# Performance work log

Hardware: AMD Instinct MI355X
Metric: run time of the kernel (lower is better)

The kernel has to match this reference:

```python
import jax, jax.numpy as jnp
import numpy as np

BLANK = 0
NEG = -1e30  # finite -inf surrogate, safe for grads
LCAP = 512   # max decoded-hypothesis label length (static shape cap)


def _ctc_single(lp, labels, T_len, L_len):
    """CTC negative log-likelihood for one sequence.
    lp: [T, V] log-probs; labels: [L] padded int labels (blank=0 excluded).
    """
    T, V = lp.shape
    L = labels.shape[0]
    S = 2 * L + 1  # extended label seq: blank interleaved
    ext = jnp.zeros((S,), jnp.int32).at[1::2].set(labels)
    ext_m2 = jnp.concatenate([jnp.full((2,), -1, jnp.int32), ext[:-2]])
    skip = (ext != BLANK) & (ext != ext_m2)  # s-2 transition allowed
    lp_ext = lp[:, ext]  # [T, S]
    alpha0 = jnp.full((S,), NEG, lp.dtype)
    alpha0 = alpha0.at[0].set(lp_ext[0, 0]).at[1].set(lp_ext[0, 1])
    neg1 = jnp.full((1,), NEG, lp.dtype)
    neg2 = jnp.full((2,), NEG, lp.dtype)

    def step(alpha, inp):
        lp_t, t = inp
        a1 = jnp.concatenate([neg1, alpha[:-1]])
        a2 = jnp.where(skip, jnp.concatenate([neg2, alpha[:-2]]), NEG)
        new = jnp.logaddexp(jnp.logaddexp(alpha, a1), a2) + lp_t
        # freeze lattice past this sequence's true length
        return jnp.where(t < T_len, new, alpha), None

    alphaT, _ = jax.lax.scan(step, alpha0, (lp_ext[1:], jnp.arange(1, T)))
    end = jnp.logaddexp(alphaT[2 * L_len], alphaT[2 * L_len - 1])
    return -end


def _ctc_batch(acts, labels, act_lens, label_lens):
    lp = jax.nn.log_softmax(acts, axis=-1)   # [T, B, V]
    lp = jnp.transpose(lp, (1, 0, 2))        # [B, T, V]
    return jax.vmap(_ctc_single)(lp, labels, act_lens, label_lens)


def _greedy_decode(acts, act_lens):
    """Greedy CTC decode: argmax, collapse repeats, drop blanks. Static shapes."""
    T, B, V = acts.shape
    preds = jnp.argmax(acts, axis=-1).T.astype(jnp.int32)  # [B, T]
    prev = jnp.concatenate([jnp.full((B, 1), -1, jnp.int32), preds[:, :-1]], axis=1)
    tix = jnp.arange(T)[None, :]
    new_tok = (preds != BLANK) & (preds != prev) & (tix < act_lens[:, None])
    pos = jnp.cumsum(new_tok, axis=1) - 1
    keep = new_tok & (pos < LCAP)
    buf = jnp.zeros((B, LCAP + 1), jnp.int32)
    buf = buf.at[jnp.arange(B)[:, None], jnp.where(keep, pos, LCAP)].set(preds)
    dec = buf[:, :LCAP]
    dec_lens = jnp.maximum(jnp.minimum(new_tok.sum(axis=1), LCAP), 1).astype(jnp.int32)
    return dec, dec_lens


def setup_inputs() -> dict:
    key = jax.random.key(0)
    k1, k2, k3, k4 = jax.random.split(key, 4)
    T, B, V, L = 1500, 96, 128, 256
    acts = jax.random.normal(k1, (T, B, V), jnp.float32)
    labels = jax.random.randint(k2, (B, L), 1, V).astype(jnp.int32)
    act_lens = jax.random.randint(k3, (B,), 800, T + 1).astype(jnp.int32)
    label_lens = jax.random.randint(k4, (B,), 64, L + 1).astype(jnp.int32)
    return {"acts": acts, "labels": labels, "act_lens": act_lens, "label_lens": label_lens}


def reference(acts, labels, act_lens, label_lens):
    aug_loss = 1.0
    dec_labels, dec_lens = _greedy_decode(acts, act_lens)
    cost_gt = _ctc_batch(acts, labels, act_lens, label_lens)
    cost_hyp = _ctc_batch(acts, dec_labels, act_lens, dec_lens)
    return cost_gt - cost_hyp + aug_loss  # [B] per-utterance hinge costs
```

## Files before the change

kernel.cpp:

```cpp
#include <hip/hip_runtime.h>

#define TT 1500
#define BB 96
#define VV 128
#define LGT 256
#define LCAP 512
#define NEGF (-1.0e30f)
#define L2E 1.4426950408889634f
#define LN2F 0.6931471805599453f
#define NW 11
#define GH 34
#define HREF 16

__global__ __launch_bounds__(256) void decode_kernel(
    const float* __restrict__ acts, const int* __restrict__ act_lens,
    int* __restrict__ dec, int* __restrict__ dec_lens) {
  __shared__ int preds[TT];
  __shared__ int sc[256];
  const int b = blockIdx.x;
  const int tid = threadIdx.x;
  const int Tl = act_lens[b];
  for (int t = tid; t < Tl; t += 256) {
    const float4* r4 = (const float4*)(acts + ((size_t)t * BB + b) * VV);
    float best = -3.4e38f;
    int bi = 0;
#pragma unroll
    for (int i = 0; i < VV / 4; i++) {
      float4 v = r4[i];
      if (v.x > best) { best = v.x; bi = 4 * i; }
      if (v.y > best) { best = v.y; bi = 4 * i + 1; }
      if (v.z > best) { best = v.z; bi = 4 * i + 2; }
      if (v.w > best) { best = v.w; bi = 4 * i + 3; }
    }
    preds[t] = bi;
  }
  __syncthreads();

  int pv[6];
  bool fl[6];
  int cnt = 0;
#pragma unroll
  for (int j = 0; j < 6; j++) {
    int t = tid * 6 + j;
    bool valid = t < Tl;
    int p = valid ? preds[t] : 0;
    int pr = (t == 0) ? -1 : (valid ? preds[t - 1] : -1);
    bool f = valid && (p != 0) && (p != pr);
    pv[j] = p;
    fl[j] = f;
    cnt += f;
  }
  sc[tid] = cnt;
  __syncthreads();
  for (int off = 1; off < 256; off <<= 1) {
    int v = sc[tid];
    if (tid >= off) v += sc[tid - off];
    __syncthreads();
    sc[tid] = v;
    __syncthreads();
  }
  int pos = sc[tid] - cnt;
  int total = sc[255];
  int* db = dec + (size_t)b * LCAP;
#pragma unroll
  for (int j = 0; j < 6; j++) {
    if (fl[j]) {
      if (pos < LCAP) db[pos] = pv[j];
      pos++;
    }
  }
  if (tid == 0) {
    if (total == 0) db[0] = 0;
    dec_lens[b] = max(1, min(total, LCAP));
  }
}

__device__ __forceinline__ float shr1_negf(float x) {
  int r = __builtin_amdgcn_update_dpp(__float_as_int(NEGF), __float_as_int(x),
                                      0x138, 0xf, 0xf, false);
  return __int_as_float(r);
}

__device__ __forceinline__ float log1p2f(float x) {
  float w = __builtin_fmaf(x, 0.6666666666666666f, -0.3333333333333333f);
  float p = -0.16666666666666666f;
  p = __builtin_fmaf(p, w, 0.2f);
  p = __builtin_fmaf(p, w, -0.25f);
  p = __builtin_fmaf(p, w, 0.3333333333333333f);
  p = __builtin_fmaf(p, w, -0.5f);
  p = __builtin_fmaf(p, w, 1.0f);
  return __builtin_fmaf(p * w, L2E, 0.5849625007211562f);
}

__global__ __launch_bounds__(64 * NW, 1) void ctc_kernel(
    const float* __restrict__ acts, const int* __restrict__ labels_gt,
    const int* __restrict__ act_lens, const int* __restrict__ label_lens,
    const int* __restrict__ dec, const int* __restrict__ dec_lens,
    float* __restrict__ ends) {
  __shared__ float xall[2][2 * LCAP + 2];
  __shared__ float fin[2];
  const int b = blockIdx.x >> 1;
  const int hyp = blockIdx.x & 1;
  const int Tl = act_lens[b];
  const int len = hyp ? dec_lens[b] : label_lens[b];
  const int* lab = hyp ? (dec + (size_t)b * LCAP) : (labels_gt + (size_t)b * LGT);
  const int S = 2 * len + 1;
  const float* act_b = acts + (size_t)b * VV;
  const int Tlm1 = Tl - 1;

  const int tid = threadIdx.x;
  const int lane = tid & 63, wv = tid >> 6;
  const int oS = 2 * ((S + 2 * NW - 1) / (2 * NW));
  const int Se = (S + 1) & ~1;
  const int o0 = min(wv * oS, Se);
  const int o1 = min(o0 + oS, S);
  const int p0 = max(0, o0 - GH);
  const int s0 = p0 + 2 * lane;
  const int s1 = s0 + 1;

  int e1 = 0;
  bool skip = false;
  if (s1 < S) {
    int li = s1 >> 1;
    e1 = lab[li];
    if (s1 >= 3) skip = (e1 != 0) && (e1 != lab[li - 1]);
  }

  float a0 = NEGF, a1 = NEGF;
  if (wv == 0 && lane == 0) {
    a0 = act_b[0] * L2E;
    a1 = act_b[e1] * L2E;
  }

  float gL0, gL1, gL2, gL3, gL4, gL5, gL6, gL7;
  float gB0, gB1, gB2, gB3, gB4, gB5, gB6, gB7;

#define PREF(GL, GB, ROW)                                  \
  {                                                        \
    const float* rp_ = act_b + (size_t)(ROW) * (BB * VV);  \
    GB = rp_[0];                                           \
    GL = rp_[e1];                                          \
  }

#define STEPK(GL, GB)                                                     \
  {                                                                       \
    float pe = shr1_negf(a1);                                             \
                              \
    float m0 = fmaxf(a0, pe);                                             \
    float d0 = fminf(a0, pe) - m0;                                        \
    float u = m0 + log1p2f(__builtin_exp2f(d0));                          \
                                  \
    float w = skip ? u : a0;                                              \
    float m1 = fmaxf(a1, w);                                              \
    float d1 = fminf(a1, w) - m1;                                         \
    float v = m1 + log1p2f(__builtin_exp2f(d1));                          \
    a0 = __builtin_fmaf(GB, L2E, u);                                      \
    a1 = __builtin_fmaf(GL, L2E, v);                                      \
  }

#define REFRESH(K)                                       \
  {                                                      \
    float* xs = xall[(K)&1];                             \
    if (s0 >= o0 && s0 < o1) xs[s0] = a0;                \
    if (s1 >= o0 && s1 < o1) xs[s1] = a1;                \
    asm volatile("s_waitcnt lgkmcnt(0)" ::: "memory");   \
    __builtin_amdgcn_s_barrier();                        \
    if (s0 < o0) {                                       \
      a0 = xs[s0];                                       \
      a1 = (s1 < S) ? xs[s1] : NEGF;                     \
    }                                                    \
  }

#define W1(OFF, GL, GB)                    \
  STEPK(GL, GB);                           \
  PREF(GL, GB, min(t + (OFF) + 8, Tlm1));

#define T1(GL, GB)                         \
  STEPK(GL, GB);                           \
  PREF(GL, GB, min(t + 8, Tlm1));          \
  ++t;                                     \
  if (t >= Tl) break;

  PREF(gL0, gB0, min(1, Tlm1));
  PREF(gL1, gB1, min(2, Tlm1));
  PREF(gL2, gB2, min(3, Tlm1));
  PREF(gL3, gB3, min(4, Tlm1));
  PREF(gL4, gB4, min(5, Tlm1));
  PREF(gL5, gB5, min(6, Tlm1));
  PREF(gL6, gB6, min(7, Tlm1));
  PREF(gL7, gB7, min(8, Tlm1));

  int t = 1, k = 0;
  while (t + HREF <= Tl) {
    W1(0, gL0, gB0)
    W1(1, gL1, gB1)
    W1(2, gL2, gB2)
    W1(3, gL3, gB3)
    W1(4, gL4, gB4)
    W1(5, gL5, gB5)
    W1(6, gL6, gB6)
    W1(7, gL7, gB7)
    W1(8, gL0, gB0)
    W1(9, gL1, gB1)
    W1(10, gL2, gB2)
    W1(11, gL3, gB3)
    W1(12, gL4, gB4)
    W1(13, gL5, gB5)
    W1(14, gL6, gB6)
    W1(15, gL7, gB7)
    t += HREF;
    ++k;
    REFRESH(k);
  }
  while (t < Tl) {
    T1(gL0, gB0)
    T1(gL1, gB1)
    T1(gL2, gB2)
    T1(gL3, gB3)
    T1(gL4, gB4)
    T1(gL5, gB5)
    T1(gL6, gB6)
    T1(gL7, gB7)
  }
#undef T1
#undef W1
#undef REFRESH
#undef STEPK
#undef PREF

  __syncthreads();
  if (s0 >= o0 && s0 < o1 && s0 == 2 * len) fin[0] = a0;
  if (s1 >= o0 && s1 < o1 && s1 == 2 * len - 1) fin[1] = a1;
  __syncthreads();
  if (tid == 0) {
    float a = fin[0], c = fin[1];
    float m = fmaxf(a, c);
    float e = m + __builtin_log2f(__builtin_exp2f(a - m) + __builtin_exp2f(c - m));
    ends[hyp * BB + b] = e;
  }
}

__global__ void final_kernel(const float* __restrict__ ends,
                             float* __restrict__ out) {
  int b = threadIdx.x;
  if (b < BB) out[b] = (ends[BB + b] - ends[b]) * LN2F + 1.0f;
}

extern "C" void kernel_launch(void* const* d_in, const int* in_sizes, int n_in,
                              void* d_out, int out_size, void* d_ws,
                              size_t ws_size, hipStream_t stream) {
  const float* acts = (const float*)d_in[0];
  const int* labels = (const int*)d_in[1];
  const int* act_lens = (const int*)d_in[2];
  const int* label_lens = (const int*)d_in[3];
  float* out = (float*)d_out;

  char* ws = (char*)d_ws;
  int* dec = (int*)ws;
  int* dec_lens = (int*)(ws + (size_t)BB * LCAP * 4);
  float* ends = (float*)(ws + (size_t)BB * LCAP * 4 + BB * 4);

  decode_kernel<<<dim3(BB), dim3(256), 0, stream>>>(acts, act_lens, dec, dec_lens);
  ctc_kernel<<<dim3(2 * BB), dim3(64 * NW), 80 * 1024, stream>>>(
      acts, labels, act_lens, label_lens, dec, dec_lens, ends);
  final_kernel<<<dim3(1), dim3(128), 0, stream>>>(ends, out);
}
```

Before: 347.9 us.

## Use 16 waves per CTC block and a shallower log-add-exp polynomial

Raises the CTC kernel from 11 to 16 waves per block, so each wave owns a narrower slice of the lattice and the serial per-wave work per timestep shrinks. The log1p polynomial is re-expressed in Estrin form with log2(e) folded into the coefficients, cutting the dependent FMA chain on the critical recurrence path. Log-add-exp now uses exp2(-|a-b|) in place of the min/max subtraction. The dynamic shared memory request drops slightly, likely to keep one block per CU. More waves mean more ghost-region overlap and a larger barrier cost per refresh.

```diff
diff --git a/kernel.cpp b/kernel.cpp
--- a/kernel.cpp
+++ b/kernel.cpp
@@ -8,7 +8,7 @@
 #define NEGF (-1.0e30f)
 #define L2E 1.4426950408889634f
 #define LN2F 0.6931471805599453f
-#define NW 11
+#define NW 16
 #define GH 34
 #define HREF 16
 
@@ -83,13 +83,20 @@
 
 __device__ __forceinline__ float log1p2f(float x) {
   float w = __builtin_fmaf(x, 0.6666666666666666f, -0.3333333333333333f);
-  float p = -0.16666666666666666f;
-  p = __builtin_fmaf(p, w, 0.2f);
-  p = __builtin_fmaf(p, w, -0.25f);
-  p = __builtin_fmaf(p, w, 0.3333333333333333f);
-  p = __builtin_fmaf(p, w, -0.5f);
-  p = __builtin_fmaf(p, w, 1.0f);
-  return __builtin_fmaf(p * w, L2E, 0.5849625007211562f);
+  float Q01 = __builtin_fmaf(w, -0.7213475204444817f, 1.4426950408889634f);
+  float Q23 = __builtin_fmaf(w, -0.36067376022224085f, 0.4808983469629878f);
+  float Q45 = __builtin_fmaf(w, -0.24044917348149392f, 0.2885390081777927f);
+  float w2 = w * w;
+  float w4 = w2 * w2;
+  float r = __builtin_fmaf(w2, Q23, Q01);
+  r = __builtin_fmaf(w4, Q45, r);
+  return __builtin_fmaf(r, w, 0.5849625007211562f);
+}
+
+__device__ __forceinline__ float lse2f(float a, float b) {
+  float m = fmaxf(a, b);
+  float x = __builtin_exp2f(-__builtin_fabsf(a - b));
+  return m + log1p2f(x);
 }
 
 __global__ __launch_bounds__(64 * NW, 1) void ctc_kernel(
@@ -145,15 +152,9 @@
 #define STEPK(GL, GB)                                                     \
   {                                                                       \
     float pe = shr1_negf(a1);                                             \
-                              \
-    float m0 = fmaxf(a0, pe);                                             \
-    float d0 = fminf(a0, pe) - m0;                                        \
-    float u = m0 + log1p2f(__builtin_exp2f(d0));                          \
-                                  \
+    float u = lse2f(a0, pe);                                              \
     float w = skip ? u : a0;                                              \
-    float m1 = fmaxf(a1, w);                                              \
-    float d1 = fminf(a1, w) - m1;                                         \
-    float v = m1 + log1p2f(__builtin_exp2f(d1));                          \
+    float v = lse2f(a1, w);                                               \
     a0 = __builtin_fmaf(GB, L2E, u);                                      \
     a1 = __builtin_fmaf(GL, L2E, v);                                      \
   }
@@ -261,7 +262,7 @@
   float* ends = (float*)(ws + (size_t)BB * LCAP * 4 + BB * 4);
 
   decode_kernel<<<dim3(BB), dim3(256), 0, stream>>>(acts, act_lens, dec, dec_lens);
-  ctc_kernel<<<dim3(2 * BB), dim3(64 * NW), 80 * 1024, stream>>>(
+  ctc_kernel<<<dim3(2 * BB), dim3(64 * NW), 76 * 1024, stream>>>(
       acts, labels, act_lens, label_lens, dec, dec_lens, ends);
   final_kernel<<<dim3(1), dim3(128), 0, stream>>>(ends, out);
 }
```

Result: slower. 439.7 us (+26.4%).

## Shorten halo refresh interval, reduce waves, reassociate log1p polynomial

Applied to the files above, without the earlier changes.

The CTC lattice kernel now exchanges halo values every 6 timesteps instead of 16, with a halo of 14 instead of 34 and 9 waves per block instead of 11. The prefetch depth also drops from 8 rows to 6. The log1p2f polynomial becomes an Estrin-style evaluation to shorten the dependent FMA chain on the serial recurrence. The smaller halo cuts redundant per-wave computation, but barriers become more frequent and fewer rows are in flight to hide global-memory latency.

```diff
diff --git a/kernel.cpp b/kernel.cpp
--- a/kernel.cpp
+++ b/kernel.cpp
@@ -8,9 +8,9 @@
 #define NEGF (-1.0e30f)
 #define L2E 1.4426950408889634f
 #define LN2F 0.6931471805599453f
-#define NW 11
-#define GH 34
-#define HREF 16
+#define NW 9
+#define GH 14
+#define HREF 6
 
 __global__ __launch_bounds__(256) void decode_kernel(
     const float* __restrict__ acts, const int* __restrict__ act_lens,
@@ -83,13 +83,15 @@
 
 __device__ __forceinline__ float log1p2f(float x) {
   float w = __builtin_fmaf(x, 0.6666666666666666f, -0.3333333333333333f);
-  float p = -0.16666666666666666f;
-  p = __builtin_fmaf(p, w, 0.2f);
-  p = __builtin_fmaf(p, w, -0.25f);
-  p = __builtin_fmaf(p, w, 0.3333333333333333f);
-  p = __builtin_fmaf(p, w, -0.5f);
-  p = __builtin_fmaf(p, w, 1.0f);
-  return __builtin_fmaf(p * w, L2E, 0.5849625007211562f);
+  float w2 = w * w;
+  float wl = w * L2E;
+  float P01 = __builtin_fmaf(w, -0.5f, 1.0f);
+  float P23 = __builtin_fmaf(w, -0.25f, 0.3333333333333333f);
+  float P45 = __builtin_fmaf(w, -0.16666666666666666f, 0.2f);
+  float w4 = w2 * w2;
+  float p = __builtin_fmaf(w2, P23, P01);
+  p = __builtin_fmaf(w4, P45, p);
+  return __builtin_fmaf(p, wl, 0.5849625007211562f);
 }
 
 __global__ __launch_bounds__(64 * NW, 1) void ctc_kernel(
@@ -132,8 +134,8 @@
     a1 = act_b[e1] * L2E;
   }
 
-  float gL0, gL1, gL2, gL3, gL4, gL5, gL6, gL7;
-  float gB0, gB1, gB2, gB3, gB4, gB5, gB6, gB7;
+  float gL0, gL1, gL2, gL3, gL4, gL5;
+  float gB0, gB1, gB2, gB3, gB4, gB5;
 
 #define PREF(GL, GB, ROW)                                  \
   {                                                        \
@@ -173,11 +175,11 @@
 
 #define W1(OFF, GL, GB)                    \
   STEPK(GL, GB);                           \
-  PREF(GL, GB, min(t + (OFF) + 8, Tlm1));
+  PREF(GL, GB, min(t + (OFF) + 6, Tlm1));
 
 #define T1(GL, GB)                         \
   STEPK(GL, GB);                           \
-  PREF(GL, GB, min(t + 8, Tlm1));          \
+  PREF(GL, GB, min(t + 6, Tlm1));          \
   ++t;                                     \
   if (t >= Tl) break;
 
@@ -187,8 +189,6 @@
   PREF(gL3, gB3, min(4, Tlm1));
   PREF(gL4, gB4, min(5, Tlm1));
   PREF(gL5, gB5, min(6, Tlm1));
-  PREF(gL6, gB6, min(7, Tlm1));
-  PREF(gL7, gB7, min(8, Tlm1));
 
   int t = 1, k = 0;
   while (t + HREF <= Tl) {
@@ -198,16 +198,6 @@
     W1(3, gL3, gB3)
     W1(4, gL4, gB4)
     W1(5, gL5, gB5)
-    W1(6, gL6, gB6)
-    W1(7, gL7, gB7)
-    W1(8, gL0, gB0)
-    W1(9, gL1, gB1)
-    W1(10, gL2, gB2)
-    W1(11, gL3, gB3)
-    W1(12, gL4, gB4)
-    W1(13, gL5, gB5)
-    W1(14, gL6, gB6)
-    W1(15, gL7, gB7)
     t += HREF;
     ++k;
     REFRESH(k);
@@ -219,8 +209,6 @@
     T1(gL3, gB3)
     T1(gL4, gB4)
     T1(gL5, gB5)
-    T1(gL6, gB6)
-    T1(gL7, gB7)
   }
 #undef T1
 #undef W1
```

After: 391.7 us. 12.6% more time.
